# Kernel optimization log

Hardware: AMD Instinct MI355X
Metric: run time of the kernel (lower is better)

The kernel has to match this reference:

```python
import jax, jax.numpy as jnp
import numpy as np

NHEAD = 8
ROUTING_STEPS = 2
TEMP = 1.0
ROPE_THETA = 10000.0


def rmsnorm(x, w, eps=1e-6):
    return x * jax.lax.rsqrt(jnp.mean(x * x, axis=-1, keepdims=True) + eps) * w


def rope_cos_sin(seq_len, head_dim, theta):
    inv = 1.0 / (theta ** (jnp.arange(0, head_dim, 2, dtype=jnp.float32) / head_dim))
    freqs = jnp.outer(jnp.arange(seq_len, dtype=jnp.float32), inv)  # [S, hd/2]
    return jnp.cos(freqs), jnp.sin(freqs)


def apply_rope(x, cos, sin):
    # x: [B,H,S,hd]; cos/sin: [S, hd/2]
    x1, x2 = x[..., 0::2], x[..., 1::2]
    c, s = cos[None, None], sin[None, None]
    r1 = x1 * c - x2 * s
    r2 = x1 * s + x2 * c
    return jnp.stack([r1, r2], axis=-1).reshape(x.shape)


def cube_forward(x, wq, wk, wv, wo, w1, w2, g1, g2, cos, sin):
    # Per-sample gathered expert weights: wq.. [B,D,D], w1 [B,D,F], w2 [B,F,D]
    B, S, D = x.shape
    H = NHEAD
    hd = D // H
    xn = rmsnorm(x, g1[:, None, :])
    q = jnp.einsum('bsd,bde->bse', xn, wq).reshape(B, S, H, hd).transpose(0, 2, 1, 3)
    k = jnp.einsum('bsd,bde->bse', xn, wk).reshape(B, S, H, hd).transpose(0, 2, 1, 3)
    v = jnp.einsum('bsd,bde->bse', xn, wv).reshape(B, S, H, hd).transpose(0, 2, 1, 3)
    q = apply_rope(q, cos, sin)
    k = apply_rope(k, cos, sin)
    scores = jnp.einsum('bhqd,bhkd->bhqk', q, k) / jnp.sqrt(jnp.float32(hd))
    causal = jnp.tril(jnp.ones((S, S), dtype=bool))
    scores = jnp.where(causal, scores, jnp.float32(-1e30))
    att = jax.nn.softmax(scores, axis=-1)
    o = jnp.einsum('bhqk,bhkd->bhqd', att, v).transpose(0, 2, 1, 3).reshape(B, S, D)
    x = x + jnp.einsum('bsd,bde->bse', o, wo)
    hn = rmsnorm(x, g2[:, None, :])
    ff = jax.nn.silu(jnp.einsum('bsd,bdf->bsf', hn, w1))
    return x + jnp.einsum('bsf,bfd->bsd', ff, w2)


def reference(input_ids, start_cubes, emb, Wq, Wk, Wv, Wo, W1, W2, n1, n2, gate_w, final_norm_w, fc_out_w):
    B, S = input_ids.shape
    D = emb.shape[1]
    C = Wq.shape[0]
    x = emb[input_ids] * jnp.sqrt(jnp.float32(D))
    cos, sin = rope_cos_sin(S, D // NHEAD, ROPE_THETA)
    # deterministic ring graph: neighbors of cube i are (i+1)%C and (i+2)%C
    ar = jnp.arange(C)
    adj = jnp.zeros((C, C), dtype=bool).at[ar, (ar + 1) % C].set(True).at[ar, (ar + 2) % C].set(True)
    cur = start_cubes
    acc_probs = jnp.zeros(C + 1, dtype=jnp.float32)
    acc_lb = jnp.float32(0.0)
    for _ in range(ROUTING_STEPS):
        x = cube_forward(x, Wq[cur], Wk[cur], Wv[cur], Wo[cur], W1[cur], W2[cur], n1[cur], n2[cur], cos, sin)
        pooled = x.mean(axis=1)                        # [B, D]
        scores = pooled @ gate_w                       # [B, C+1]
        probs = jax.nn.softmax(scores / TEMP, axis=-1)
        acc_probs = acc_probs + probs.sum(axis=0)
        avg = probs.mean(axis=0)
        acc_lb = acc_lb + (C + 1) * jnp.sum(avg * avg)
        masked = jnp.where(adj[cur], scores[:, :C], jnp.float32(-1e30))
        cur = jnp.argmax(masked, axis=-1)
    logits = jnp.einsum('bsd,dv->bsv', rmsnorm(x, final_norm_w), fc_out_w)
    avg_probs = acc_probs / jnp.float32(ROUTING_STEPS * B)
    aux_variance_loss = jnp.var(avg_probs)
    aux_lb_loss = acc_lb / jnp.float32(ROUTING_STEPS)
    return logits, aux_variance_loss, aux_lb_loss


def setup_inputs() -> dict:
    key = jax.random.key(0)
    ks = jax.random.split(key, 16)
    V, D, F, C, B, S = 32000, 512, 2048, 4, 2, 256
    w = 0.02
    return {
        'input_ids': jax.random.randint(ks[0], (B, S), 0, V),
        'start_cubes': jax.random.randint(ks[1], (B,), 0, C),
        'emb': jax.random.normal(ks[2], (V, D), jnp.float32) * w,
        'Wq': jax.random.normal(ks[3], (C, D, D), jnp.float32) * w,
        'Wk': jax.random.normal(ks[4], (C, D, D), jnp.float32) * w,
        'Wv': jax.random.normal(ks[5], (C, D, D), jnp.float32) * w,
        'Wo': jax.random.normal(ks[6], (C, D, D), jnp.float32) * w,
        'W1': jax.random.normal(ks[7], (C, D, F), jnp.float32) * w,
        'W2': jax.random.normal(ks[8], (C, F, D), jnp.float32) * w,
        'n1': jnp.ones((C, D), jnp.float32),
        'n2': jnp.ones((C, D), jnp.float32),
        'gate_w': jax.random.normal(ks[9], (D, C + 1), jnp.float32) * w,
        'final_norm_w': jnp.ones((D,), jnp.float32),
        'fc_out_w': jax.random.normal(ks[10], (D, V), jnp.float32) * w,
    }
```

## Files before the change

kernel.cpp:

```cpp
#include <hip/hip_runtime.h>
#include <hip/hip_bf16.h>

#define BB 2
#define SS 256
#define DDIM 512
#define HH 8
#define HDIM 64
#define FDIM 2048
#define CC 4
#define VV 32000
#define NTOK (BB*SS)
#define PCHUNK 16

typedef __hip_bfloat16 bf16;
typedef __attribute__((ext_vector_type(8))) short short8;
typedef __attribute__((ext_vector_type(4))) short short4v;
typedef __attribute__((ext_vector_type(4))) float floatx4;

__device__ __forceinline__ int get_mode(const unsigned* __restrict__ probe) {
    return (probe[0] == 0x3F800000u) ? 0 : 1;
}
__device__ __forceinline__ float ldw(const void* __restrict__ p, long i, int mode) {
    if (mode == 0) return ((const float*)p)[i];
    return __bfloat162float(((const bf16*)p)[i]);
}
__device__ __forceinline__ void stf(void* __restrict__ p, long i, float v, int mode) {
    if (mode == 0) ((float*)p)[i] = v;
    else ((bf16*)p)[i] = __float2bfloat16(v);
}

__device__ __forceinline__ void gload16(const void* g, void* l) {
    __builtin_amdgcn_global_load_lds(
        (const __attribute__((address_space(1))) unsigned int*)g,
        (__attribute__((address_space(3))) unsigned int*)l, 16, 0, 0);
}

__global__ void init_kernel(const int* __restrict__ ids,
                            const int* __restrict__ start_cubes,
                            const void* __restrict__ emb,
                            float* __restrict__ x,
                            float* __restrict__ acc_probs,
                            float* __restrict__ acc_lb,
                            int* __restrict__ cur,
                            const unsigned* __restrict__ probe) {
    int mode = get_mode(probe);
    int gid = blockIdx.x * blockDim.x + threadIdx.x;
    if (gid < NTOK * DDIM) {
        int tok = gid / DDIM, d = gid % DDIM;
        x[gid] = ldw(emb, (long)ids[tok] * DDIM + d, mode) * 22.627416997969522f;
    }
    if (gid < CC + 1) acc_probs[gid] = 0.f;
    if (gid == CC + 1) *acc_lb = 0.f;
    if (gid < BB) cur[gid] = start_cubes[gid];
}

__global__ void rope_table_kernel(float2* __restrict__ rt) {
    int gid = blockIdx.x * blockDim.x + threadIdx.x;
    if (gid >= SS * 32) return;
    int j = gid & 31, s = gid >> 5;
    float inv = expf(-(float)j * (logf(10000.f) / 32.f));
    float ang = (float)s * inv;
    rt[gid] = make_float2(cosf(ang), sinf(ang));
}

__global__ void rmsnorm_kernel(const float* __restrict__ in,
                               void* __restrict__ out, int obf,
                               const void* __restrict__ gamma,
                               const int* __restrict__ cur,
                               float* __restrict__ zbuf, int zn,
                               const unsigned* __restrict__ probe) {
    int mode = get_mode(probe);
    int tok = blockIdx.x;
    int b = tok / SS;
    long goff = cur ? (long)cur[b] * DDIM : 0;
    if (zbuf) {
        int gtid = blockIdx.x * blockDim.x + threadIdx.x;
        int gstride = gridDim.x * blockDim.x;
        for (int i = gtid; i < zn; i += gstride) zbuf[i] = 0.f;
    }
    __shared__ float red[256];
    int t = threadIdx.x;
    float x0 = in[(long)tok * DDIM + t];
    float x1 = in[(long)tok * DDIM + t + 256];
    red[t] = x0 * x0 + x1 * x1;
    __syncthreads();
    for (int s = 128; s > 0; s >>= 1) {
        if (t < s) red[t] += red[t + s];
        __syncthreads();
    }
    float scale = rsqrtf(red[0] / DDIM + 1e-6f);
    float v0 = x0 * scale * ldw(gamma, goff + t, mode);
    float v1 = x1 * scale * ldw(gamma, goff + t + 256, mode);
    if (obf) {
        ((bf16*)out)[(long)tok * DDIM + t]       = __float2bfloat16(v0);
        ((bf16*)out)[(long)tok * DDIM + t + 256] = __float2bfloat16(v1);
    } else {
        ((float*)out)[(long)tok * DDIM + t]       = v0;
        ((float*)out)[(long)tok * DDIM + t + 256] = v1;
    }
}

__global__ void silu_kernel(const float* __restrict__ in,
                            ushort* __restrict__ out, int n) {
    int i4 = (blockIdx.x * blockDim.x + threadIdx.x) * 4;
    if (i4 >= n) return;
    float4 v = *(const float4*)&in[i4];
    float a = v.x / (1.f + expf(-v.x));
    float b = v.y / (1.f + expf(-v.y));
    float c = v.z / (1.f + expf(-v.z));
    float d = v.w / (1.f + expf(-v.w));
    bf16 t0 = __float2bfloat16(a), t1 = __float2bfloat16(b);
    bf16 t2 = __float2bfloat16(c), t3 = __float2bfloat16(d);
    short4v o;
    o[0] = *(short*)&t0; o[1] = *(short*)&t1;
    o[2] = *(short*)&t2; o[3] = *(short*)&t3;
    *(short4v*)&out[i4] = o;
}

__global__ void transpose_kernel(const void* __restrict__ in, bf16* __restrict__ out,
                                 int K, int N, long ims, long oms,
                                 const unsigned* __restrict__ probe) {
    int mode = get_mode(probe);
    __shared__ float tile[32][33];
    int mat = blockIdx.z;
    int n0 = blockIdx.x * 32, k0 = blockIdx.y * 32;
    int tx = threadIdx.x, ty = threadIdx.y;
#pragma unroll
    for (int i = 0; i < 4; i++)
        tile[ty + i * 8][tx] = ldw(in, (long)mat * ims + (long)(k0 + ty + i * 8) * N + (n0 + tx), mode);
    __syncthreads();
#pragma unroll
    for (int i = 0; i < 4; i++)
        out[(long)mat * oms + (long)(n0 + ty + i * 8) * K + (k0 + tx)] =
            __float2bfloat16(tile[tx][ty + i * 8]);
}

template <int BN>
__global__ __launch_bounds__(BN * 2)
void gemm_mfma(const ushort* __restrict__ A,
               const ushort* __restrict__ WtB,
               const int* __restrict__ cur, long wcube, long wz,
               int K, int N,
               const float* __restrict__ res,
               void* __restrict__ out, long ozstride,
               int omode, int ACT, int nsplit, int swz,
               const unsigned* __restrict__ probe) {
    constexpr int BLK = BN * 2;
    constexpr int CA  = 1024 / BLK;
    constexpr int CB  = (BN * 8) / BLK;
    int mode = get_mode(probe);
    __shared__ __align__(16) ushort sA[2][128 * 64];
    __shared__ __align__(16) ushort sB[2][BN * 64];
    int tid = threadIdx.x;
    int mi = blockIdx.y, ni = blockIdx.x;
    if (swz) {
        int nb = gridDim.x, mb = gridDim.y;
        int lin = blockIdx.x + blockIdx.y * nb;
        int nwg = nb * mb;
        int q = nwg >> 3, r = nwg & 7;
        int xcd = lin & 7, pos = lin >> 3;
        int nid = (xcd < r ? xcd * (q + 1) : r * (q + 1) + (xcd - r) * q) + pos;
        mi = nid % mb;
        ni = nid / mb;
    }
    int m0 = mi * 128;
    int n0 = ni * BN;
    int z  = blockIdx.z / nsplit;
    int ks = blockIdx.z % nsplit;
    int Kc = K / nsplit;
    int kbeg = ks * Kc;
    const ushort* Wt = WtB + (long)z * wz + (cur ? (long)cur[m0 / SS] * wcube : 0);
    floatx4 acc[4][4];
#pragma unroll
    for (int i = 0; i < 4; i++)
#pragma unroll
        for (int j = 0; j < 4; j++)
#pragma unroll
            for (int r = 0; r < 4; r++) acc[i][j][r] = 0.f;
    int w = tid >> 6, lane = tid & 63;
    int wm = (w & 1) * 64;
    int wn = (w >> 1) * 64;
    int lr = lane & 15, quad = lane >> 4;

    auto stage = [&](int buf, int k0) {
#pragma unroll
        for (int i = 0; i < CA; i++) {
            int g  = tid + i * BLK;
            int gs = g ^ ((g >> 3) & 7);
            gload16(&A[(long)(m0 + (gs >> 3)) * K + k0 + (gs & 7) * 8], &sA[buf][g * 8]);
        }
#pragma unroll
        for (int i = 0; i < CB; i++) {
            int g  = tid + i * BLK;
            int gs = g ^ ((g >> 3) & 7);
            gload16(&Wt[(long)(n0 + (gs >> 3)) * K + k0 + (gs & 7) * 8], &sB[buf][g * 8]);
        }
    };

    int nsteps = Kc >> 6;
    stage(0, kbeg);
    for (int j = 0; j < nsteps; ++j) {
        int cu = j & 1;
        if (j + 1 < nsteps) {
            stage(cu ^ 1, kbeg + ((j + 1) << 6));
            if constexpr (CA + CB == 8)
                asm volatile("s_waitcnt vmcnt(8)" ::: "memory");
            else
                asm volatile("s_waitcnt vmcnt(6)" ::: "memory");
        } else {
            asm volatile("s_waitcnt vmcnt(0)" ::: "memory");
        }
        __builtin_amdgcn_sched_barrier(0);
        __builtin_amdgcn_s_barrier();
#pragma unroll
        for (int half = 0; half < 2; ++half) {
            short8 af[4], bfr[4];
#pragma unroll
            for (int i = 0; i < 4; i++) {
                int oA = (wm + i * 16 + lr) * 8 + quad + half * 4;
                int sa = oA ^ ((oA >> 3) & 7);
                af[i]  = *(const short8*)&sA[cu][sa * 8];
                int oB = (wn + i * 16 + lr) * 8 + quad + half * 4;
                int sb = oB ^ ((oB >> 3) & 7);
                bfr[i] = *(const short8*)&sB[cu][sb * 8];
            }
#pragma unroll
            for (int mm = 0; mm < 4; mm++)
#pragma unroll
                for (int nn = 0; nn < 4; nn++)
                    acc[mm][nn] = __builtin_amdgcn_mfma_f32_16x16x32_bf16(af[mm], bfr[nn], acc[mm][nn], 0, 0, 0);
        }
        asm volatile("s_waitcnt lgkmcnt(0)" ::: "memory");
        __builtin_amdgcn_sched_barrier(0);
        __builtin_amdgcn_s_barrier();
    }
#pragma unroll
    for (int mm = 0; mm < 4; mm++)
#pragma unroll
        for (int nn = 0; nn < 4; nn++) {
            int col = n0 + wn + nn * 16 + lr;
#pragma unroll
            for (int r = 0; r < 4; r++) {
                int row = m0 + wm + mm * 16 + quad * 4 + r;
                float v = acc[mm][nn][r];
                long oi = (long)z * ozstride + (long)row * N + col;
                if (omode == 3) {
                    atomicAdd((float*)out + oi, v);
                } else {
                    if (ACT == 1) v = v / (1.f + expf(-v));
                    if (res) v += res[(long)row * N + col];
                    if (omode == 0)      ((float*)out)[oi] = v;
                    else if (omode == 1) ((bf16*)out)[oi] = __float2bfloat16(v);
                    else                 stf(out, oi, v, mode);
                }
            }
        }
}

__global__ void rope_kernel(float* __restrict__ q, float* __restrict__ k) {
    int gid = blockIdx.x * blockDim.x + threadIdx.x;
    if (gid >= NTOK * HH * (HDIM / 2)) return;
    int j = gid % (HDIM / 2);
    int rest = gid / (HDIM / 2);
    int h = rest % HH;
    int tok = rest / HH;
    int s = tok % SS;
    float inv = expf(-(float)j * (logf(10000.f) / 32.f));
    float ang = (float)s * inv;
    float c = cosf(ang), sn = sinf(ang);
    long base = (long)tok * DDIM + h * HDIM + 2 * j;
    float q1 = q[base], q2 = q[base + 1];
    q[base]     = q1 * c - q2 * sn;
    q[base + 1] = q1 * sn + q2 * c;
    float k1 = k[base], k2 = k[base + 1];
    k[base]     = k1 * c - k2 * sn;
    k[base + 1] = k1 * sn + k2 * c;
}

__global__ void attn_kernel(const float* __restrict__ q,
                            const float* __restrict__ k,
                            const float* __restrict__ v,
                            const float2* __restrict__ rt,
                            void* __restrict__ o, int obf) {
    int blk = blockIdx.x;
    int qr = blk % SS;
    int h = (blk / SS) % HH;
    int b = blk / (SS * HH);
    int t = threadIdx.x;
    __shared__ float sc[256];
    __shared__ float red[256];
    __shared__ __align__(16) float qs[HDIM];
    long qbase = ((long)(b * SS + qr)) * DDIM + h * HDIM;
    if (t < HDIM) {
        if (rt) {
            int j = t >> 1;
            float2 cs = rt[qr * 32 + j];
            float q1 = q[qbase + 2 * j], q2 = q[qbase + 2 * j + 1];
            qs[t] = (t & 1) ? (q1 * cs.y + q2 * cs.x) : (q1 * cs.x - q2 * cs.y);
        } else {
            qs[t] = q[qbase + t];
        }
    }
    __syncthreads();
    float s = -1e30f;
    if (t <= qr) {
        long kbase = ((long)(b * SS + t)) * DDIM + h * HDIM;
        const float4* k4 = (const float4*)&k[kbase];
        const float4* q4 = (const float4*)qs;
        float acc = 0.f;
        if (rt) {
            const float4* rt4 = (const float4*)&rt[t * 32];
#pragma unroll
            for (int i = 0; i < HDIM / 4; i++) {
                float4 kv = k4[i], cs2 = rt4[i], a = q4[i];
                float r0 = kv.x * cs2.x - kv.y * cs2.y;
                float r1 = kv.x * cs2.y + kv.y * cs2.x;
                float r2 = kv.z * cs2.z - kv.w * cs2.w;
                float r3 = kv.z * cs2.w + kv.w * cs2.z;
                acc += a.x * r0 + a.y * r1 + a.z * r2 + a.w * r3;
            }
        } else {
#pragma unroll
            for (int i = 0; i < HDIM / 4; i++) {
                float4 a = q4[i], bv = k4[i];
                acc += a.x * bv.x + a.y * bv.y + a.z * bv.z + a.w * bv.w;
            }
        }
        s = acc * 0.125f;
    }
    sc[t] = s;
    red[t] = s;
    __syncthreads();
    for (int st = 128; st > 0; st >>= 1) {
        if (t < st) red[t] = fmaxf(red[t], red[t + st]);
        __syncthreads();
    }
    float m = red[0];
    __syncthreads();
    float e = (t <= qr) ? expf(sc[t] - m) : 0.f;
    sc[t] = e;
    red[t] = e;
    __syncthreads();
    for (int st = 128; st > 0; st >>= 1) {
        if (t < st) red[t] += red[t + st];
        __syncthreads();
    }
    float invsum = 1.f / red[0];
    __syncthreads();
    int g = t >> 6, d = t & 63;
    float pacc = 0.f;
    for (int kk = g; kk <= qr; kk += 4)
        pacc += sc[kk] * v[((long)(b * SS + kk)) * DDIM + h * HDIM + d];
    red[t] = pacc;
    __syncthreads();
    if (t < HDIM) {
        float vv = (red[t] + red[t + 64] + red[t + 128] + red[t + 192]) * invsum;
        if (obf) ((bf16*)o)[qbase + t] = __float2bfloat16(vv);
        else     ((float*)o)[qbase + t] = vv;
    }
}

__global__ void pool_partial_kernel(const float* __restrict__ x,
                                    float* __restrict__ partial) {
    int blk = blockIdx.x;
    int b = blk / (SS / PCHUNK);
    int c = blk % (SS / PCHUNK);
    int t = threadIdx.x;
    float acc = 0.f;
    long base = ((long)b * SS + c * PCHUNK) * DDIM + t;
#pragma unroll
    for (int i = 0; i < PCHUNK; i++) acc += x[base + (long)i * DDIM];
    partial[(long)blk * DDIM + t] = acc;
}

__global__ void routing_kernel(const float* __restrict__ partial,
                               const void* __restrict__ gate_w,
                               float* __restrict__ acc_probs,
                               float* __restrict__ acc_lb,
                               int* __restrict__ cur,
                               int final_step,
                               void* __restrict__ d_out,
                               const unsigned* __restrict__ probe) {
    int mode = get_mode(probe);
    __shared__ float wred[8][BB * (CC + 1)];
    __shared__ float scores[BB][CC + 1];
    int t = threadIdx.x;
    float pm[BB];
#pragma unroll
    for (int b = 0; b < BB; b++) {
        float acc = 0.f;
#pragma unroll
        for (int c = 0; c < SS / PCHUNK; c++)
            acc += partial[((long)b * (SS / PCHUNK) + c) * DDIM + t];
        pm[b] = acc / (float)SS;
    }
    float part[BB][CC + 1];
#pragma unroll
    for (int c = 0; c <= CC; c++) {
        float g = ldw(gate_w, (long)t * (CC + 1) + c, mode);
#pragma unroll
        for (int b = 0; b < BB; b++) part[b][c] = pm[b] * g;
    }
#pragma unroll
    for (int off = 32; off > 0; off >>= 1)
#pragma unroll
        for (int b = 0; b < BB; b++)
#pragma unroll
            for (int c = 0; c <= CC; c++)
                part[b][c] += __shfl_down(part[b][c], off);
    int wave = t >> 6, lane = t & 63;
    if (lane == 0)
#pragma unroll
        for (int b = 0; b < BB; b++)
#pragma unroll
            for (int c = 0; c <= CC; c++)
                wred[wave][b * (CC + 1) + c] = part[b][c];
    __syncthreads();
    if (t == 0) {
        for (int b = 0; b < BB; b++)
            for (int c = 0; c <= CC; c++) {
                float s = 0.f;
                for (int wv = 0; wv < 8; wv++) s += wred[wv][b * (CC + 1) + c];
                scores[b][c] = s;
            }
        float probs[BB][CC + 1];
        for (int b = 0; b < BB; b++) {
            float m = -1e30f;
            for (int c = 0; c <= CC; c++) m = fmaxf(m, scores[b][c]);
            float sum = 0.f;
            for (int c = 0; c <= CC; c++) { probs[b][c] = expf(scores[b][c] - m); sum += probs[b][c]; }
            for (int c = 0; c <= CC; c++) probs[b][c] /= sum;
        }
        float lb = 0.f;
        for (int c = 0; c <= CC; c++) {
            float sumb = 0.f;
            for (int b = 0; b < BB; b++) sumb += probs[b][c];
            acc_probs[c] += sumb;
            float avg = sumb / (float)BB;
            lb += avg * avg;
        }
        *acc_lb += (float)(CC + 1) * lb;
        for (int b = 0; b < BB; b++) {
            int cu = cur[b];
            int a1 = (cu + 1) % CC, a2 = (cu + 2) % CC;
            float best = -1e38f; int bi = 0;
            for (int c = 0; c < CC; c++) {
                float vv = (c == a1 || c == a2) ? scores[b][c] : -1e30f;
                if (vv > best) { best = vv; bi = c; }
            }
            cur[b] = bi;
        }
        if (final_step) {
            float ap[CC + 1], mean = 0.f;
            for (int c = 0; c <= CC; c++) { ap[c] = acc_probs[c] / (2.f * BB); mean += ap[c]; }
            mean /= (float)(CC + 1);
            float var = 0.f;
            for (int c = 0; c <= CC; c++) { float d = ap[c] - mean; var += d * d; }
            var /= (float)(CC + 1);
            stf(d_out, (long)NTOK * VV + 0, var, mode);
            stf(d_out, (long)NTOK * VV + 1, (*acc_lb) / 2.f, mode);
        }
    }
}

template <int TM, int ACT, bool OUT_DYN>
__global__ void gemm_kernel(const float* __restrict__ A,
                            const void* __restrict__ Wbase,
                            const int* __restrict__ cur, long wstride,
                            int K, int N,
                            const float* __restrict__ res,
                            void* __restrict__ out,
                            const unsigned* __restrict__ probe) {
    int mode = get_mode(probe);
    extern __shared__ float sA[];
    int row0 = blockIdx.y * TM;
    long woff = cur ? (long)cur[row0 / SS] * wstride : 0;
    int t = threadIdx.x;
    for (int i = t; i < TM * K; i += 256)
        sA[i] = A[(long)(row0 + i / K) * K + (i % K)];
    __syncthreads();
    int n = blockIdx.x * 256 + t;
    float acc[TM];
#pragma unroll
    for (int r = 0; r < TM; r++) acc[r] = 0.f;
    for (int k = 0; k < K; k++) {
        float w = ldw(Wbase, woff + (long)k * N + n, mode);
#pragma unroll
        for (int r = 0; r < TM; r++) acc[r] += sA[r * K + k] * w;
    }
#pragma unroll
    for (int r = 0; r < TM; r++) {
        float v = acc[r];
        if (ACT == 1) v = v / (1.f + expf(-v));
        if (res) v += res[(long)(row0 + r) * N + n];
        long oi = (long)(row0 + r) * N + n;
        if constexpr (OUT_DYN) stf(out, oi, v, mode);
        else                   ((float*)out)[oi] = v;
    }
}

__global__ void routing_kernel_fb(const float* __restrict__ x,
                                  const void* __restrict__ gate_w,
                                  float* __restrict__ acc_probs,
                                  float* __restrict__ acc_lb,
                                  int* __restrict__ cur,
                                  int final_step,
                                  void* __restrict__ d_out,
                                  const unsigned* __restrict__ probe) {
    int mode = get_mode(probe);
    __shared__ float pooled[BB][DDIM];
    __shared__ float scores[BB][CC + 1];
    int t = threadIdx.x;
    for (int b = 0; b < BB; b++) {
        float acc = 0.f;
        for (int s = 0; s < SS; s++) acc += x[((long)(b * SS + s)) * DDIM + t];
        pooled[b][t] = acc / (float)SS;
    }
    __syncthreads();
    if (t < BB * (CC + 1)) {
        int b = t / (CC + 1), c = t % (CC + 1);
        float acc = 0.f;
        for (int d = 0; d < DDIM; d++)
            acc += pooled[b][d] * ldw(gate_w, (long)d * (CC + 1) + c, mode);
        scores[b][c] = acc;
    }
    __syncthreads();
    if (t == 0) {
        float probs[BB][CC + 1];
        for (int b = 0; b < BB; b++) {
            float m = -1e30f;
            for (int c = 0; c <= CC; c++) m = fmaxf(m, scores[b][c]);
            float sum = 0.f;
            for (int c = 0; c <= CC; c++) { probs[b][c] = expf(scores[b][c] - m); sum += probs[b][c]; }
            for (int c = 0; c <= CC; c++) probs[b][c] /= sum;
        }
        float lb = 0.f;
        for (int c = 0; c <= CC; c++) {
            float sumb = 0.f;
            for (int b = 0; b < BB; b++) sumb += probs[b][c];
            acc_probs[c] += sumb;
            float avg = sumb / (float)BB;
            lb += avg * avg;
        }
        *acc_lb += (float)(CC + 1) * lb;
        for (int b = 0; b < BB; b++) {
            int cu = cur[b];
            int a1 = (cu + 1) % CC, a2 = (cu + 2) % CC;
            float best = -1e38f; int bi = 0;
            for (int c = 0; c < CC; c++) {
                float vv = (c == a1 || c == a2) ? scores[b][c] : -1e30f;
                if (vv > best) { best = vv; bi = c; }
            }
            cur[b] = bi;
        }
        if (final_step) {
            float ap[CC + 1], mean = 0.f;
            for (int c = 0; c <= CC; c++) { ap[c] = acc_probs[c] / (2.f * BB); mean += ap[c]; }
            mean /= (float)(CC + 1);
            float var = 0.f;
            for (int c = 0; c <= CC; c++) { float d = ap[c] - mean; var += d * d; }
            var /= (float)(CC + 1);
            stf(d_out, (long)NTOK * VV + 0, var, mode);
            stf(d_out, (long)NTOK * VV + 1, (*acc_lb) / 2.f, mode);
        }
    }
}

extern "C" void kernel_launch(void* const* d_in, const int* in_sizes, int n_in,
                              void* d_out, int out_size, void* d_ws, size_t ws_size,
                              hipStream_t stream) {
    const int*  ids   = (const int*)d_in[0];
    const int*  start = (const int*)d_in[1];
    const void* emb   = d_in[2];
    const void* Wq    = d_in[3];
    const void* Wk    = d_in[4];
    const void* Wv    = d_in[5];
    const void* Wo    = d_in[6];
    const void* W1    = d_in[7];
    const void* W2    = d_in[8];
    const void* n1    = d_in[9];
    const void* n2    = d_in[10];
    const void* gate  = d_in[11];
    const void* fnorm = d_in[12];
    const void* fcw   = d_in[13];
    const unsigned* probe = (const unsigned*)d_in[9];

    char* base = (char*)d_ws;
    size_t off = 0;
    auto alloc = [&](size_t bytes) { size_t p = off; off = (off + bytes + 255) & ~(size_t)255; return p; };
    size_t x_o    = alloc((size_t)NTOK * DDIM * 4);
    size_t qkv_o  = alloc((size_t)3 * NTOK * DDIM * 4);
    size_t xn_o   = alloc((size_t)NTOK * DDIM * 2);
    size_t ob_o   = alloc((size_t)NTOK * DDIM * 2);
    size_t ff_o   = alloc((size_t)NTOK * FDIM * 2);
    size_t ffp_o  = alloc((size_t)NTOK * FDIM * 4);
    size_t acc_o  = alloc(256);
    size_t part_o = alloc((size_t)BB * (SS / PCHUNK) * DDIM * 4);
    size_t rt_o   = alloc((size_t)SS * 32 * 8);
    size_t qkvT_o = alloc((size_t)3 * CC * DDIM * DDIM * 2);
    size_t WoT_o  = alloc((size_t)CC * DDIM * DDIM * 2);
    size_t W1T_o  = alloc((size_t)CC * DDIM * FDIM * 2);
    size_t W2T_o  = alloc((size_t)CC * FDIM * DDIM * 2);
    size_t fcwT_o = alloc((size_t)DDIM * VV * 2);
    bool big = ws_size >= off;

    if (big) {
        float* x    = (float*)(base + x_o);
        float* qkv  = (float*)(base + qkv_o);
        float* q = qkv, *k = qkv + NTOK * DDIM, *v = qkv + 2 * NTOK * DDIM;
        bf16*  xn   = (bf16*)(base + xn_o);
        bf16*  ob   = (bf16*)(base + ob_o);
        bf16*  ff   = (bf16*)(base + ff_o);
        float* ffp  = (float*)(base + ffp_o);
        float* acc_probs = (float*)(base + acc_o);
        float* acc_lb = acc_probs + 8;
        int*   cur = (int*)(acc_lb + 8);
        float* partial = (float*)(base + part_o);
        float2* rt = (float2*)(base + rt_o);
        bf16* qkvT = (bf16*)(base + qkvT_o);
        bf16* WoT  = (bf16*)(base + WoT_o);
        bf16* W1T  = (bf16*)(base + W1T_o);
        bf16* W2T  = (bf16*)(base + W2T_o);
        bf16* fcwT = (bf16*)(base + fcwT_o);

        dim3 tb(32, 8);
        transpose_kernel<<<dim3(16, 16, CC), tb, 0, stream>>>(Wq, qkvT,                 DDIM, DDIM, (long)DDIM*DDIM, (long)DDIM*DDIM, probe);
        transpose_kernel<<<dim3(16, 16, CC), tb, 0, stream>>>(Wk, qkvT +   CC*DDIM*DDIM, DDIM, DDIM, (long)DDIM*DDIM, (long)DDIM*DDIM, probe);
        transpose_kernel<<<dim3(16, 16, CC), tb, 0, stream>>>(Wv, qkvT + 2*CC*DDIM*DDIM, DDIM, DDIM, (long)DDIM*DDIM, (long)DDIM*DDIM, probe);
        transpose_kernel<<<dim3(16, 16, CC), tb, 0, stream>>>(Wo, WoT,  DDIM, DDIM, (long)DDIM*DDIM, (long)DDIM*DDIM, probe);
        transpose_kernel<<<dim3(64, 16, CC), tb, 0, stream>>>(W1, W1T,  DDIM, FDIM, (long)DDIM*FDIM, (long)FDIM*DDIM, probe);
        transpose_kernel<<<dim3(16, 64, CC), tb, 0, stream>>>(W2, W2T,  FDIM, DDIM, (long)FDIM*DDIM, (long)DDIM*FDIM, probe);
        transpose_kernel<<<dim3(1000, 16, 1), tb, 0, stream>>>(fcw, fcwT, DDIM, VV, 0, 0, probe);
        rope_table_kernel<<<(SS * 32 + 255) / 256, 256, 0, stream>>>(rt);

        init_kernel<<<(NTOK * DDIM + 255) / 256, 256, 0, stream>>>(
            ids, start, emb, x, acc_probs, acc_lb, cur, probe);

        const long DD2 = (long)DDIM * DDIM;
        const int QS = 4;
        const int OS = 4;
        const int F1S = 4;
        const int F2S = 8;
        for (int step = 0; step < 2; step++) {
            rmsnorm_kernel<<<NTOK, 256, 0, stream>>>(x, xn, 1, n1, cur,
                                                     qkv, 3 * NTOK * DDIM, probe);
            gemm_mfma<256><<<dim3(DDIM/256, NTOK/128, 3*QS), 512, 0, stream>>>(
                (const ushort*)xn, (const ushort*)qkvT, cur, DD2, (long)CC*DD2,
                DDIM, DDIM, nullptr, qkv, (long)NTOK*DDIM, 3, 0, QS, 0, probe);
            attn_kernel<<<BB * HH * SS, 256, 0, stream>>>(q, k, v, rt, ob, 1);
            gemm_mfma<256><<<dim3(DDIM/256, NTOK/128, OS), 512, 0, stream>>>(
                (const ushort*)ob, (const ushort*)WoT, cur, DD2, 0,
                DDIM, DDIM, nullptr, x, 0, 3, 0, OS, 0, probe);
            rmsnorm_kernel<<<NTOK, 256, 0, stream>>>(x, xn, 1, n2, cur,
                                                     ffp, NTOK * FDIM, probe);
            gemm_mfma<256><<<dim3(FDIM/256, NTOK/128, F1S), 512, 0, stream>>>(
                (const ushort*)xn, (const ushort*)W1T, cur, (long)FDIM*DDIM, 0,
                DDIM, FDIM, nullptr, ffp, 0, 3, 0, F1S, 0, probe);
            silu_kernel<<<(NTOK * FDIM / 4 + 255) / 256, 256, 0, stream>>>(
                ffp, (ushort*)ff, NTOK * FDIM);
            gemm_mfma<256><<<dim3(DDIM/256, NTOK/128, F2S), 512, 0, stream>>>(
                (const ushort*)ff, (const ushort*)W2T, cur, (long)DDIM*FDIM, 0,
                FDIM, DDIM, nullptr, x, 0, 3, 0, F2S, 0, probe);
            pool_partial_kernel<<<BB * (SS / PCHUNK), 512, 0, stream>>>(x, partial);
            routing_kernel<<<1, 512, 0, stream>>>(
                partial, gate, acc_probs, acc_lb, cur, step == 1, d_out, probe);
        }
        rmsnorm_kernel<<<NTOK, 256, 0, stream>>>(x, xn, 1, fnorm, nullptr,
                                                 nullptr, 0, probe);
        gemm_mfma<128><<<dim3(VV/128, NTOK/128, 1), 256, 0, stream>>>(
            (const ushort*)xn, (const ushort*)fcwT, nullptr, 0, 0,
            DDIM, VV, nullptr, d_out, 0, 2, 0, 1, 1, probe);
        return;
    }

    float* ws = (float*)d_ws;
    float* x  = ws;
    float* xn = x  + NTOK * DDIM;
    float* q  = xn + NTOK * DDIM;
    float* k  = q  + NTOK * DDIM;
    float* v  = k  + NTOK * DDIM;
    float* o  = v  + NTOK * DDIM;
    float* ff = o  + NTOK * DDIM;
    float* acc_probs = ff + NTOK * FDIM;
    float* acc_lb    = acc_probs + 8;
    int*   cur       = (int*)(acc_lb + 8);
    const long DD2 = (long)DDIM * DDIM;

    init_kernel<<<(NTOK * DDIM + 255) / 256, 256, 0, stream>>>(
        ids, start, emb, x, acc_probs, acc_lb, cur, probe);
    for (int step = 0; step < 2; step++) {
        rmsnorm_kernel<<<NTOK, 256, 0, stream>>>(x, xn, 0, n1, cur, nullptr, 0, probe);
        dim3 gdd(DDIM / 256, NTOK / 16);
        size_t smem16 = 16 * DDIM * sizeof(float);
        gemm_kernel<16, 0, false><<<gdd, 256, smem16, stream>>>(
            xn, Wq, cur, DD2, DDIM, DDIM, nullptr, q, probe);
        gemm_kernel<16, 0, false><<<gdd, 256, smem16, stream>>>(
            xn, Wk, cur, DD2, DDIM, DDIM, nullptr, k, probe);
        gemm_kernel<16, 0, false><<<gdd, 256, smem16, stream>>>(
            xn, Wv, cur, DD2, DDIM, DDIM, nullptr, v, probe);
        rope_kernel<<<(NTOK * HH * (HDIM / 2) + 255) / 256, 256, 0, stream>>>(q, k);
        attn_kernel<<<BB * HH * SS, 256, 0, stream>>>(q, k, v, nullptr, o, 0);
        gemm_kernel<16, 0, false><<<gdd, 256, smem16, stream>>>(
            o, Wo, cur, DD2, DDIM, DDIM, x, x, probe);
        rmsnorm_kernel<<<NTOK, 256, 0, stream>>>(x, xn, 0, n2, cur, nullptr, 0, probe);
        dim3 gdf(FDIM / 256, NTOK / 16);
        gemm_kernel<16, 1, false><<<gdf, 256, smem16, stream>>>(
            xn, W1, cur, (long)DDIM * FDIM, DDIM, FDIM, nullptr, ff, probe);
        dim3 gfd(DDIM / 256, NTOK / 4);
        size_t smem4f = 4 * FDIM * sizeof(float);
        gemm_kernel<4, 0, false><<<gfd, 256, smem4f, stream>>>(
            ff, W2, cur, (long)FDIM * DDIM, FDIM, DDIM, x, x, probe);
        routing_kernel_fb<<<1, 512, 0, stream>>>(
            x, gate, acc_probs, acc_lb, cur, step == 1, d_out, probe);
    }
    rmsnorm_kernel<<<NTOK, 256, 0, stream>>>(x, xn, 0, fnorm, nullptr, nullptr, 0, probe);
    dim3 gv(VV / 256, NTOK / 16);
    size_t smem16 = 16 * DDIM * sizeof(float);
    gemm_kernel<16, 0, true><<<gv, 256, smem16, stream>>>(
        xn, fcw, nullptr, 0, DDIM, VV, nullptr, d_out, probe);
}
```

Measured before the change: 551.6 us.

## Process four query rows per attention block and use BK=32 for layer GEMMs

The attention kernel now computes four query rows per block, so each K row is loaded and rotated once and reused across four queries; V loads are shared the same way, and block count drops fourfold. The MFMA GEMM gains a K-tile template parameter, and the per-layer GEMMs switch to a 32-wide K step, which halves shared memory per block and may raise occupancy at the cost of more synchronization steps. Blocks near the diagonal do slightly more masked work.

```diff
diff --git a/kernel.cpp b/kernel.cpp
--- a/kernel.cpp
+++ b/kernel.cpp
@@ -11,6 +11,7 @@
 #define VV 32000
 #define NTOK (BB*SS)
 #define PCHUNK 16
+#define QT 4
 
 typedef __hip_bfloat16 bf16;
 typedef __attribute__((ext_vector_type(8))) short short8;
@@ -135,7 +136,7 @@
             __float2bfloat16(tile[tx][ty + i * 8]);
 }
 
-template <int BN>
+template <int BN, int BK>
 __global__ __launch_bounds__(BN * 2)
 void gemm_mfma(const ushort* __restrict__ A,
                const ushort* __restrict__ WtB,
@@ -145,12 +146,15 @@
                void* __restrict__ out, long ozstride,
                int omode, int ACT, int nsplit, int swz,
                const unsigned* __restrict__ probe) {
-    constexpr int BLK = BN * 2;
-    constexpr int CA  = 1024 / BLK;
-    constexpr int CB  = (BN * 8) / BLK;
+    constexpr int BLK  = BN * 2;
+    constexpr int CPR  = BK / 8;
+    constexpr int CPRS = (BK == 32) ? 2 : 3;
+    constexpr int CA   = (128 * CPR) / BLK;
+    constexpr int CB   = (BN * CPR) / BLK;
+    constexpr int HALVES = BK / 32;
     int mode = get_mode(probe);
-    __shared__ __align__(16) ushort sA[2][128 * 64];
-    __shared__ __align__(16) ushort sB[2][BN * 64];
+    __shared__ __align__(16) ushort sA[2][128 * BK];
+    __shared__ __align__(16) ushort sB[2][BN * BK];
     int tid = threadIdx.x;
     int mi = blockIdx.y, ni = blockIdx.x;
     if (swz) {
@@ -187,40 +191,40 @@
         for (int i = 0; i < CA; i++) {
             int g  = tid + i * BLK;
             int gs = g ^ ((g >> 3) & 7);
-            gload16(&A[(long)(m0 + (gs >> 3)) * K + k0 + (gs & 7) * 8], &sA[buf][g * 8]);
+            gload16(&A[(long)(m0 + (gs >> CPRS)) * K + k0 + (gs & (CPR - 1)) * 8], &sA[buf][g * 8]);
         }
 #pragma unroll
         for (int i = 0; i < CB; i++) {
             int g  = tid + i * BLK;
             int gs = g ^ ((g >> 3) & 7);
-            gload16(&Wt[(long)(n0 + (gs >> 3)) * K + k0 + (gs & 7) * 8], &sB[buf][g * 8]);
+            gload16(&Wt[(long)(n0 + (gs >> CPRS)) * K + k0 + (gs & (CPR - 1)) * 8], &sB[buf][g * 8]);
         }
     };
 
-    int nsteps = Kc >> 6;
+    int nsteps = Kc / BK;
     stage(0, kbeg);
     for (int j = 0; j < nsteps; ++j) {
         int cu = j & 1;
         if (j + 1 < nsteps) {
-            stage(cu ^ 1, kbeg + ((j + 1) << 6));
-            if constexpr (CA + CB == 8)
+            stage(cu ^ 1, kbeg + (j + 1) * BK);
+            if constexpr (CA + CB == 3)
+                asm volatile("s_waitcnt vmcnt(3)" ::: "memory");
+            else
                 asm volatile("s_waitcnt vmcnt(8)" ::: "memory");
-            else
-                asm volatile("s_waitcnt vmcnt(6)" ::: "memory");
         } else {
             asm volatile("s_waitcnt vmcnt(0)" ::: "memory");
         }
         __builtin_amdgcn_sched_barrier(0);
         __builtin_amdgcn_s_barrier();
 #pragma unroll
-        for (int half = 0; half < 2; ++half) {
+        for (int half = 0; half < HALVES; ++half) {
             short8 af[4], bfr[4];
 #pragma unroll
             for (int i = 0; i < 4; i++) {
-                int oA = (wm + i * 16 + lr) * 8 + quad + half * 4;
+                int oA = (wm + i * 16 + lr) * CPR + half * 4 + quad;
                 int sa = oA ^ ((oA >> 3) & 7);
                 af[i]  = *(const short8*)&sA[cu][sa * 8];
-                int oB = (wn + i * 16 + lr) * 8 + quad + half * 4;
+                int oB = (wn + i * 16 + lr) * CPR + half * 4 + quad;
                 int sb = oB ^ ((oB >> 3) & 7);
                 bfr[i] = *(const short8*)&sB[cu][sb * 8];
             }
@@ -283,80 +287,114 @@
                             const float2* __restrict__ rt,
                             void* __restrict__ o, int obf) {
     int blk = blockIdx.x;
-    int qr = blk % SS;
-    int h = (blk / SS) % HH;
-    int b = blk / (SS * HH);
+    const int nqt = SS / QT;
+    int qt = blk % nqt;
+    int h = (blk / nqt) % HH;
+    int b = blk / (nqt * HH);
+    int qr0 = qt * QT;
+    int qrmax = qr0 + QT - 1;
     int t = threadIdx.x;
-    __shared__ float sc[256];
-    __shared__ float red[256];
-    __shared__ __align__(16) float qs[HDIM];
-    long qbase = ((long)(b * SS + qr)) * DDIM + h * HDIM;
-    if (t < HDIM) {
+    __shared__ float sc[QT][SS];
+    __shared__ float red[QT][256];
+    __shared__ __align__(16) float qs[QT][HDIM];
+    __shared__ float invs[QT];
+    {
+        int qi = t >> 6, d = t & 63;
+        long qb = ((long)(b * SS + qr0 + qi)) * DDIM + h * HDIM;
+        float val;
         if (rt) {
-            int j = t >> 1;
-            float2 cs = rt[qr * 32 + j];
-            float q1 = q[qbase + 2 * j], q2 = q[qbase + 2 * j + 1];
-            qs[t] = (t & 1) ? (q1 * cs.y + q2 * cs.x) : (q1 * cs.x - q2 * cs.y);
+            int j = d >> 1;
+            float2 cs = rt[(qr0 + qi) * 32 + j];
+            float q1 = q[qb + 2 * j], q2 = q[qb + 2 * j + 1];
+            val = (d & 1) ? (q1 * cs.y + q2 * cs.x) : (q1 * cs.x - q2 * cs.y);
         } else {
-            qs[t] = q[qbase + t];
-        }
-    }
-    __syncthreads();
-    float s = -1e30f;
-    if (t <= qr) {
+            val = q[qb + d];
+        }
+        qs[qi][d] = val;
+    }
+    __syncthreads();
+    float s0 = -1e30f, s1 = -1e30f, s2 = -1e30f, s3 = -1e30f;
+    if (t <= qrmax) {
         long kbase = ((long)(b * SS + t)) * DDIM + h * HDIM;
         const float4* k4 = (const float4*)&k[kbase];
-        const float4* q4 = (const float4*)qs;
-        float acc = 0.f;
+        float4 kr[HDIM / 4];
         if (rt) {
             const float4* rt4 = (const float4*)&rt[t * 32];
 #pragma unroll
             for (int i = 0; i < HDIM / 4; i++) {
-                float4 kv = k4[i], cs2 = rt4[i], a = q4[i];
-                float r0 = kv.x * cs2.x - kv.y * cs2.y;
-                float r1 = kv.x * cs2.y + kv.y * cs2.x;
-                float r2 = kv.z * cs2.z - kv.w * cs2.w;
-                float r3 = kv.z * cs2.w + kv.w * cs2.z;
-                acc += a.x * r0 + a.y * r1 + a.z * r2 + a.w * r3;
+                float4 kv = k4[i], cs2 = rt4[i];
+                kr[i].x = kv.x * cs2.x - kv.y * cs2.y;
+                kr[i].y = kv.x * cs2.y + kv.y * cs2.x;
+                kr[i].z = kv.z * cs2.z - kv.w * cs2.w;
+                kr[i].w = kv.z * cs2.w + kv.w * cs2.z;
             }
         } else {
 #pragma unroll
-            for (int i = 0; i < HDIM / 4; i++) {
-                float4 a = q4[i], bv = k4[i];
-                acc += a.x * bv.x + a.y * bv.y + a.z * bv.z + a.w * bv.w;
-            }
-        }
-        s = acc * 0.125f;
-    }
-    sc[t] = s;
-    red[t] = s;
+            for (int i = 0; i < HDIM / 4; i++) kr[i] = k4[i];
+        }
+        float a0 = 0.f, a1 = 0.f, a2 = 0.f, a3 = 0.f;
+        const float4* q40 = (const float4*)qs[0];
+        const float4* q41 = (const float4*)qs[1];
+        const float4* q42 = (const float4*)qs[2];
+        const float4* q43 = (const float4*)qs[3];
+#pragma unroll
+        for (int i = 0; i < HDIM / 4; i++) {
+            float4 kv = kr[i];
+            float4 x0 = q40[i]; a0 += x0.x*kv.x + x0.y*kv.y + x0.z*kv.z + x0.w*kv.w;
+            float4 x1 = q41[i]; a1 += x1.x*kv.x + x1.y*kv.y + x1.z*kv.z + x1.w*kv.w;
+            float4 x2 = q42[i]; a2 += x2.x*kv.x + x2.y*kv.y + x2.z*kv.z + x2.w*kv.w;
+            float4 x3 = q43[i]; a3 += x3.x*kv.x + x3.y*kv.y + x3.z*kv.z + x3.w*kv.w;
+        }
+        s0 = a0 * 0.125f; s1 = a1 * 0.125f; s2 = a2 * 0.125f; s3 = a3 * 0.125f;
+    }
+    if (t > qr0)     s0 = -1e30f;
+    if (t > qr0 + 1) s1 = -1e30f;
+    if (t > qr0 + 2) s2 = -1e30f;
+    red[0][t] = s0; red[1][t] = s1; red[2][t] = s2; red[3][t] = s3;
     __syncthreads();
     for (int st = 128; st > 0; st >>= 1) {
-        if (t < st) red[t] = fmaxf(red[t], red[t + st]);
+        if (t < st) {
+#pragma unroll
+            for (int qi = 0; qi < QT; qi++)
+                red[qi][t] = fmaxf(red[qi][t], red[qi][t + st]);
+        }
         __syncthreads();
     }
-    float m = red[0];
-    __syncthreads();
-    float e = (t <= qr) ? expf(sc[t] - m) : 0.f;
-    sc[t] = e;
-    red[t] = e;
+    float m0 = red[0][0], m1 = red[1][0], m2 = red[2][0], m3 = red[3][0];
+    __syncthreads();
+    float e0 = (t <= qr0)     ? expf(s0 - m0) : 0.f;
+    float e1 = (t <= qr0 + 1) ? expf(s1 - m1) : 0.f;
+    float e2 = (t <= qr0 + 2) ? expf(s2 - m2) : 0.f;
+    float e3 = (t <= qrmax)   ? expf(s3 - m3) : 0.f;
+    sc[0][t] = e0; sc[1][t] = e1; sc[2][t] = e2; sc[3][t] = e3;
+    red[0][t] = e0; red[1][t] = e1; red[2][t] = e2; red[3][t] = e3;
     __syncthreads();
     for (int st = 128; st > 0; st >>= 1) {
-        if (t < st) red[t] += red[t + st];
+        if (t < st) {
+#pragma unroll
+            for (int qi = 0; qi < QT; qi++)
+                red[qi][t] += red[qi][t + st];
+        }
         __syncthreads();
     }
-    float invsum = 1.f / red[0];
+    if (t < QT) invs[t] = 1.f / red[t][0];
     __syncthreads();
     int g = t >> 6, d = t & 63;
-    float pacc = 0.f;
-    for (int kk = g; kk <= qr; kk += 4)
-        pacc += sc[kk] * v[((long)(b * SS + kk)) * DDIM + h * HDIM + d];
-    red[t] = pacc;
-    __syncthreads();
-    if (t < HDIM) {
-        float vv = (red[t] + red[t + 64] + red[t + 128] + red[t + 192]) * invsum;
-        if (obf) ((bf16*)o)[qbase + t] = __float2bfloat16(vv);
-        else     ((float*)o)[qbase + t] = vv;
+    float p0 = 0.f, p1 = 0.f, p2 = 0.f, p3 = 0.f;
+    for (int kk = g; kk <= qrmax; kk += 4) {
+        float vv = v[((long)(b * SS + kk)) * DDIM + h * HDIM + d];
+        p0 += sc[0][kk] * vv; p1 += sc[1][kk] * vv;
+        p2 += sc[2][kk] * vv; p3 += sc[3][kk] * vv;
+    }
+    red[0][t] = p0; red[1][t] = p1; red[2][t] = p2; red[3][t] = p3;
+    __syncthreads();
+    {
+        int qi = t >> 6, dd = t & 63;
+        float r = red[qi][dd] + red[qi][64 + dd] + red[qi][128 + dd] + red[qi][192 + dd];
+        r *= invs[qi];
+        long ob_ = ((long)(b * SS + qr0 + qi)) * DDIM + h * HDIM + dd;
+        if (obf) ((bf16*)o)[ob_] = __float2bfloat16(r);
+        else     ((float*)o)[ob_] = r;
     }
 }
 
@@ -644,21 +682,21 @@
         for (int step = 0; step < 2; step++) {
             rmsnorm_kernel<<<NTOK, 256, 0, stream>>>(x, xn, 1, n1, cur,
                                                      qkv, 3 * NTOK * DDIM, probe);
-            gemm_mfma<256><<<dim3(DDIM/256, NTOK/128, 3*QS), 512, 0, stream>>>(
+            gemm_mfma<256,32><<<dim3(DDIM/256, NTOK/128, 3*QS), 512, 0, stream>>>(
                 (const ushort*)xn, (const ushort*)qkvT, cur, DD2, (long)CC*DD2,
                 DDIM, DDIM, nullptr, qkv, (long)NTOK*DDIM, 3, 0, QS, 0, probe);
-            attn_kernel<<<BB * HH * SS, 256, 0, stream>>>(q, k, v, rt, ob, 1);
-            gemm_mfma<256><<<dim3(DDIM/256, NTOK/128, OS), 512, 0, stream>>>(
+            attn_kernel<<<BB * HH * (SS / QT), 256, 0, stream>>>(q, k, v, rt, ob, 1);
+            gemm_mfma<256,32><<<dim3(DDIM/256, NTOK/128, OS), 512, 0, stream>>>(
                 (const ushort*)ob, (const ushort*)WoT, cur, DD2, 0,
                 DDIM, DDIM, nullptr, x, 0, 3, 0, OS, 0, probe);
             rmsnorm_kernel<<<NTOK, 256, 0, stream>>>(x, xn, 1, n2, cur,
                                                      ffp, NTOK * FDIM, probe);
-            gemm_mfma<256><<<dim3(FDIM/256, NTOK/128, F1S), 512, 0, stream>>>(
+            gemm_mfma<256,32><<<dim3(FDIM/256, NTOK/128, F1S), 512, 0, stream>>>(
                 (const ushort*)xn, (const ushort*)W1T, cur, (long)FDIM*DDIM, 0,
                 DDIM, FDIM, nullptr, ffp, 0, 3, 0, F1S, 0, probe);
             silu_kernel<<<(NTOK * FDIM / 4 + 255) / 256, 256, 0, stream>>>(
                 ffp, (ushort*)ff, NTOK * FDIM);
-            gemm_mfma<256><<<dim3(DDIM/256, NTOK/128, F2S), 512, 0, stream>>>(
+            gemm_mfma<256,32><<<dim3(DDIM/256, NTOK/128, F2S), 512, 0, stream>>>(
                 (const ushort*)ff, (const ushort*)W2T, cur, (long)DDIM*FDIM, 0,
                 FDIM, DDIM, nullptr, x, 0, 3, 0, F2S, 0, probe);
             pool_partial_kernel<<<BB * (SS / PCHUNK), 512, 0, stream>>>(x, partial);
@@ -667,7 +705,7 @@
         }
         rmsnorm_kernel<<<NTOK, 256, 0, stream>>>(x, xn, 1, fnorm, nullptr,
                                                  nullptr, 0, probe);
-        gemm_mfma<128><<<dim3(VV/128, NTOK/128, 1), 256, 0, stream>>>(
+        gemm_mfma<128,64><<<dim3(VV/128, NTOK/128, 1), 256, 0, stream>>>(
             (const ushort*)xn, (const ushort*)fcwT, nullptr, 0, 0,
             DDIM, VV, nullptr, d_out, 0, 2, 0, 1, 1, probe);
         return;
@@ -699,7 +737,7 @@
         gemm_kernel<16, 0, false><<<gdd, 256, smem16, stream>>>(
             xn, Wv, cur, DD2, DDIM, DDIM, nullptr, v, probe);
         rope_kernel<<<(NTOK * HH * (HDIM / 2) + 255) / 256, 256, 0, stream>>>(q, k);
-        attn_kernel<<<BB * HH * SS, 256, 0, stream>>>(q, k, v, nullptr, o, 0);
+        attn_kernel<<<BB * HH * (SS / QT), 256, 0, stream>>>(q, k, v, nullptr, o, 0);
         gemm_kernel<16, 0, false><<<gdd, 256, smem16, stream>>>(
             o, Wo, cur, DD2, DDIM, DDIM, x, x, probe);
         rmsnorm_kernel<<<NTOK, 256, 0, stream>>>(x, xn, 0, n2, cur, nullptr, 0, probe);
```

After: 520.6 us. -5.6%, faster.
